# Optimization experiments

Hardware: AMD Instinct MI355X
Metric: run time of the kernel (lower is better)

The kernel has to match this reference:

```python
import jax, jax.numpy as jnp
import numpy as np

IMG, P, C = 512, 16, 1
D, DEPTH, H, DH, MLP = 768, 12, 8, 64, 2048
GRID = IMG // P          # 32
NP = GRID * GRID         # 1024 patches
N = NP + 1               # +cls token
EPS = 1e-5


def _ln(x, s, b):
    m = jnp.mean(x, -1, keepdims=True)
    v = jnp.mean((x - m) ** 2, -1, keepdims=True)
    return (x - m) * jax.lax.rsqrt(v + EPS) * s + b


def setup_inputs() -> dict:
    key = jax.random.key(0)
    ks = jax.random.split(key, 12)
    s = 0.02
    f32 = jnp.float32
    return {
        "x": jax.random.normal(ks[0], (4, C, IMG, IMG), f32),
        "conv_w": jax.random.normal(ks[1], (D, C, P, P), f32) * s,   # [out,in,kh,kw] like torch
        "conv_b": jnp.zeros((D,), f32),
        "cls_token": jax.random.normal(ks[2], (1, 1, D), f32),
        "pos_emb": jax.random.normal(ks[3], (1, N, D), f32),
        "qkv_w": jax.random.normal(ks[4], (DEPTH, D, 3 * H * DH), f32) * s,  # [in,out] layout
        "merge_w": jax.random.normal(ks[5], (DEPTH, H * DH, D), f32) * s,
        "merge_b": jnp.zeros((DEPTH, D), f32),
        "ln1_s": jnp.ones((DEPTH, D), f32),
        "ln1_b": jnp.zeros((DEPTH, D), f32),
        "ln2_s": jnp.ones((DEPTH, D), f32),
        "ln2_b": jnp.zeros((DEPTH, D), f32),
        "ffn_w1": jax.random.normal(ks[6], (DEPTH, D, MLP), f32) * s,
        "ffn_b1": jnp.zeros((DEPTH, MLP), f32),
        "ffn_w2": jax.random.normal(ks[7], (DEPTH, MLP, D), f32) * s,
        "ffn_b2": jnp.zeros((DEPTH, D), f32),
        "lnf_s": jnp.ones((D,), f32),
        "lnf_b": jnp.zeros((D,), f32),
    }


def reference(x, conv_w, conv_b, cls_token, pos_emb, qkv_w, merge_w, merge_b,
              ln1_s, ln1_b, ln2_s, ln2_b, ffn_w1, ffn_b1, ffn_w2, ffn_b2,
              lnf_s, lnf_b):
    B = x.shape[0]
    # Patch embed: stride-P conv == non-overlapping patch extraction + matmul
    xr = x.reshape(B, C, GRID, P, GRID, P)
    tok = jnp.einsum('bchpwq,dcpq->bhwd', xr, conv_w).reshape(B, NP, D) + conv_b
    t = jnp.concatenate([jnp.broadcast_to(cls_token, (B, 1, D)), tok], axis=1)
    t = t + pos_emb  # dropout is identity in eval
    scale = DH ** -0.5
    for i in range(DEPTH):
        # MSA with pre-LN
        h = _ln(t, ln1_s[i], ln1_b[i])
        qkv = (h @ qkv_w[i]).reshape(B, N, H, 3, DH)   # [B,N,H,3,DH]
        q = jnp.transpose(qkv[..., 0, :], (0, 2, 1, 3))  # [B,H,N,DH]
        k = jnp.transpose(qkv[..., 1, :], (0, 2, 1, 3))
        v = jnp.transpose(qkv[..., 2, :], (0, 2, 1, 3))
        att = jax.nn.softmax(jnp.einsum('bhnd,bhmd->bhnm', q, k) * scale, axis=-1)
        o = jnp.einsum('bhnm,bhmd->bhnd', att, v)
        o = jnp.transpose(o, (0, 2, 1, 3)).reshape(B, N, H * DH)
        t = t + (o @ merge_w[i] + merge_b[i])
        # FFN with pre-LN, exact (erf) GELU like torch nn.GELU
        h2 = _ln(t, ln2_s[i], ln2_b[i])
        f = jax.nn.gelu(h2 @ ffn_w1[i] + ffn_b1[i], approximate=False)
        t = t + (f @ ffn_w2[i] + ffn_b2[i])
    return _ln(t, lnf_s, lnf_b)
```

## Files before the change

kernel.cpp:

```cpp
#include <hip/hip_runtime.h>

#define DEV __device__ __forceinline__

typedef short s8v __attribute__((ext_vector_type(8)));
typedef float f4v __attribute__((ext_vector_type(4)));

DEV short f2bf(float f) {
  unsigned u = __float_as_uint(f);
  u += 0x7FFFu + ((u >> 16) & 1u);
  return (short)(u >> 16);
}
DEV short f2bf_fast(float f) {
  return (short)((__float_as_uint(f) + 0x8000u) >> 16);
}
DEV float bf2f(short s) { return __uint_as_float(((unsigned)(unsigned short)s) << 16); }

DEV void gld_lds16(const short* g, short* l) {
  __builtin_amdgcn_global_load_lds(
      (const __attribute__((address_space(1))) void*)g,
      (__attribute__((address_space(3))) void*)l, 16, 0, 0);
}

DEV int xcd_swz(int id, int nwg) {
  int q8 = nwg >> 3, r8 = nwg & 7, xcd = id & 7, off = id >> 3;
  return (xcd < r8) ? (xcd * (q8 + 1) + off) : (r8 * (q8 + 1) + (xcd - r8) * q8 + off);
}

template<int BN>
__global__ __launch_bounds__(256) void gemm_t(
    const short* __restrict__ A, const short* __restrict__ B, void* __restrict__ Cv,
    const float* __restrict__ bias,
    int M, int N, int K, int lda, int ldb, int ldc, int flags)
{
  constexpr int BPASS = BN / 32;
  constexpr int MI = (BN == 128) ? 4 : 2;
  __shared__ __align__(16) short As[2][64 * 64];
  __shared__ __align__(16) short Bs[2][BN * 64];
  int nwg = gridDim.x * gridDim.y;
  int idl = blockIdx.y * gridDim.x + blockIdx.x;
  int swz = xcd_swz(idl, nwg);
  int bx = swz % gridDim.x, by = swz / gridDim.x;
  int m0 = by * 64, n0 = bx * BN;
  int tid = threadIdx.x, lane = tid & 63, w = tid >> 6;
  int lr = lane & 15, kg = lane >> 4;
  int wrb = (BN == 128) ? 0 : (w >> 1) * 32;
  int wcb = (BN == 128) ? w * 32 : (w & 1) * 32;
  f4v acc[MI][2] = {};
  int NT = K >> 6;

#define STAGE(bufi, k0)                                                   \
  {                                                                       \
    _Pragma("unroll")                                                     \
    for (int p = 0; p < 2; ++p) {                                         \
      int ch = p * 256 + w * 64 + lane;                                   \
      int row = ch >> 3, c = (ch & 7) ^ (row & 7);                        \
      gld_lds16(A + (long)(m0 + row) * lda + (k0) + c * 8,                \
                &As[bufi][(p * 256 + w * 64) * 8]);                       \
    }                                                                     \
    _Pragma("unroll")                                                     \
    for (int p = 0; p < BPASS; ++p) {                                     \
      int ch = p * 256 + w * 64 + lane;                                   \
      int row = ch >> 3, c = (ch & 7) ^ (row & 7);                        \
      gld_lds16(B + (long)(n0 + row) * ldb + (k0) + c * 8,                \
                &Bs[bufi][(p * 256 + w * 64) * 8]);                       \
    }                                                                     \
  }

  STAGE(0, 0)
  for (int t = 0; t < NT; ++t) {
    int buf = t & 1;
    if (t + 1 < NT) {
      STAGE(buf ^ 1, (t + 1) * 64)
      if constexpr (BN == 128)
        asm volatile("s_waitcnt vmcnt(6)" ::: "memory");
      else
        asm volatile("s_waitcnt vmcnt(4)" ::: "memory");
    } else {
      asm volatile("s_waitcnt vmcnt(0)" ::: "memory");
    }
    __builtin_amdgcn_s_barrier();
    #pragma unroll
    for (int ks = 0; ks < 2; ++ks) {
      s8v av[MI], bv[2];
      #pragma unroll
      for (int mi = 0; mi < MI; ++mi) {
        int row = wrb + mi * 16 + lr;
        int sl = (ks * 4 + kg) ^ (row & 7);
        av[mi] = *(const s8v*)&As[buf][row * 64 + sl * 8];
      }
      #pragma unroll
      for (int ni = 0; ni < 2; ++ni) {
        int row = wcb + ni * 16 + lr;
        int sl = (ks * 4 + kg) ^ (row & 7);
        bv[ni] = *(const s8v*)&Bs[buf][row * 64 + sl * 8];
      }
      #pragma unroll
      for (int mi = 0; mi < MI; ++mi)
        #pragma unroll
        for (int ni = 0; ni < 2; ++ni)
          acc[mi][ni] = __builtin_amdgcn_mfma_f32_16x16x32_bf16(av[mi], bv[ni], acc[mi][ni], 0, 0, 0);
    }
    asm volatile("s_waitcnt lgkmcnt(0)" ::: "memory");
    __builtin_amdgcn_s_barrier();
  }
#undef STAGE

  float* Cf = (float*)Cv;
  short* Cb = (short*)Cv;
  #pragma unroll
  for (int mi = 0; mi < MI; ++mi)
    #pragma unroll
    for (int ni = 0; ni < 2; ++ni) {
      int col = n0 + wcb + ni * 16 + lr;
      float bvv = (flags & 1) ? bias[col] : 0.f;
      #pragma unroll
      for (int j = 0; j < 4; ++j) {
        int row = m0 + wrb + mi * 16 + kg * 4 + j;
        if (row >= M) continue;
        float v = acc[mi][ni][j] + bvv;
        if (flags & 2) v = 0.5f * v * (1.f + erff(v * 0.70710678118f));
        long ci = (long)row * ldc + col;
        if (flags & 8) Cb[ci] = f2bf(v);
        else { if (flags & 4) v += Cf[ci]; Cf[ci] = v; }
      }
    }
}

__global__ __launch_bounds__(256) void flash_k(
    const short* __restrict__ qkv, short* __restrict__ O)
{
  int swz = xcd_swz(blockIdx.x, 544);
  int z = swz / 17, qt = swz - z * 17;
  int zb = z >> 3, zh = z & 7;
  const short* base = qkv + (long)zb * 1025 * 1536 + zh * 192;
  const short* Qg = base;
  const short* Kg = base + 64;
  const short* Vg = base + 128;
  int q0 = qt * 64;
  int tid = threadIdx.x, lane = tid & 63, w = tid >> 6;
  int lr = lane & 15, kg = lane >> 4;

  __shared__ __align__(16) short Ks[2][64 * 64];
  __shared__ __align__(16) short Vt[2][64][72];

  s8v aq[2];
  {
    long qrow = q0 + w * 16 + lr;
    aq[0] = *(const s8v*)(Qg + qrow * 1536 + kg * 8);
    aq[1] = *(const s8v*)(Qg + qrow * 1536 + 32 + kg * 8);
  }

#define STAGE_K(bufi, kv0)                                                 \
  {                                                                        \
    int s0 = w * 128;                                                      \
    _Pragma("unroll")                                                      \
    for (int i = 0; i < 2; ++i) {                                          \
      int s = s0 + i * 64 + lane;                                          \
      int row = s >> 3, c = (s & 7) ^ (row & 7);                           \
      gld_lds16(Kg + (long)((kv0) + row) * 1536 + c * 8,                   \
                &Ks[bufi][(s0 + i * 64) * 8]);                             \
    }                                                                      \
  }

  f4v acc[4] = {};
  float m_run = -3.0e38f, l_run = 0.f;
  const float C2 = 0.18033688011112042f;

  STAGE_K(0, 0)
  #pragma unroll
  for (int p = 0; p < 2; ++p) {
    int s = p * 256 + tid;
    int key = s & 63, ch = s >> 6;
    s8v v = *(const s8v*)(Vg + (long)key * 1536 + ch * 8);
    #pragma unroll
    for (int j = 0; j < 8; ++j) Vt[0][ch * 8 + j][key] = v[j];
  }
  asm volatile("s_waitcnt vmcnt(0)" ::: "memory");
  asm volatile("s_waitcnt lgkmcnt(0)" ::: "memory");
  __builtin_amdgcn_s_barrier();

  for (int kt = 0; kt < 17; ++kt) {
    int cur = kt & 1;
    int kv0 = kt * 64;
    s8v vreg[2];
    int vok[2];
    if (kt < 16) {
      STAGE_K(cur ^ 1, kv0 + 64)
      #pragma unroll
      for (int p = 0; p < 2; ++p) {
        int s = p * 256 + tid;
        int key = (s & 63) + kv0 + 64, ch = s >> 6;
        vok[p] = key < 1025;
        vreg[p] = vok[p] ? *(const s8v*)(Vg + (long)key * 1536 + ch * 8) : s8v{};
      }
    }

    f4v sa[4] = {};
    __builtin_amdgcn_s_setprio(1);
    #pragma unroll
    for (int ni = 0; ni < 4; ++ni) {
      int row = ni * 16 + lr;
      #pragma unroll
      for (int ks = 0; ks < 2; ++ks) {
        int c = (ks * 4 + kg) ^ (row & 7);
        s8v kf = *(const s8v*)&Ks[cur][row * 64 + c * 8];
        sa[ni] = __builtin_amdgcn_mfma_f32_16x16x32_bf16(kf, aq[ks], sa[ni], 0, 0, 0);
      }
    }
    __builtin_amdgcn_s_setprio(0);

    float sv[4][4], pv[4][4];
    float tm = -3.0e38f;
    if (kt != 16) {
      #pragma unroll
      for (int ni = 0; ni < 4; ++ni)
        #pragma unroll
        for (int jj = 0; jj < 4; ++jj) {
          float s = sa[ni][jj] * C2;
          sv[ni][jj] = s;
          tm = fmaxf(tm, s);
        }
    } else {
      #pragma unroll
      for (int ni = 0; ni < 4; ++ni)
        #pragma unroll
        for (int jj = 0; jj < 4; ++jj) sv[ni][jj] = -3.0e38f;
      if (kg == 0) sv[0][0] = sa[0][0] * C2;
      tm = sv[0][0];
    }
    tm = fmaxf(tm, __shfl_xor(tm, 16));
    tm = fmaxf(tm, __shfl_xor(tm, 32));
    float m_new = fmaxf(m_run, tm);
    float scale = exp2f(m_run - m_new);
    m_run = m_new;
    float ts = 0.f;
    #pragma unroll
    for (int ni = 0; ni < 4; ++ni)
      #pragma unroll
      for (int jj = 0; jj < 4; ++jj) {
        float p = exp2f(sv[ni][jj] - m_new);
        pv[ni][jj] = p;
        ts += p;
      }
    ts += __shfl_xor(ts, 16);
    ts += __shfl_xor(ts, 32);
    l_run = l_run * scale + ts;

    float scq[4];
    #pragma unroll
    for (int jj = 0; jj < 4; ++jj)
      scq[jj] = __shfl(scale, kg * 4 + jj + 16 * kg);
    #pragma unroll
    for (int ni = 0; ni < 4; ++ni)
      #pragma unroll
      for (int jj = 0; jj < 4; ++jj) acc[ni][jj] *= scq[jj];

    if (kt < 16) {
      #pragma unroll
      for (int p = 0; p < 2; ++p) {
        int s = p * 256 + tid;
        int key = s & 63, ch = s >> 6;
        s8v v = vok[p] ? vreg[p] : s8v{};
        #pragma unroll
        for (int j = 0; j < 8; ++j) Vt[cur ^ 1][ch * 8 + j][key] = v[j];
      }
    }

    unsigned pr[4][2];
    #pragma unroll
    for (int ni = 0; ni < 4; ++ni)
      #pragma unroll
      for (int h = 0; h < 2; ++h) {
        unsigned lo = (unsigned)(unsigned short)f2bf_fast(pv[ni][2 * h]);
        unsigned hi = (unsigned)(unsigned short)f2bf_fast(pv[ni][2 * h + 1]);
        pr[ni][h] = lo | (hi << 16);
      }
    union PU { s8v v; unsigned u[4]; };
    PU apu[2];
    #pragma unroll
    for (int ks = 0; ks < 2; ++ks)
      #pragma unroll
      for (int t = 0; t < 4; ++t) {
        unsigned src = (kg & 2) ? pr[2 * ks + 1][t & 1] : pr[2 * ks][t & 1];
        apu[ks].u[t] = __shfl(src, lr + 16 * (2 * (kg & 1) + (t >> 1)));
      }

    __builtin_amdgcn_s_setprio(1);
    #pragma unroll
    for (int ni = 0; ni < 4; ++ni) {
      #pragma unroll
      for (int ks = 0; ks < 2; ++ks) {
        s8v bvv = *(const s8v*)&Vt[cur][ni * 16 + lr][ks * 32 + kg * 8];
        acc[ni] = __builtin_amdgcn_mfma_f32_16x16x32_bf16(apu[ks].v, bvv, acc[ni], 0, 0, 0);
      }
    }
    __builtin_amdgcn_s_setprio(0);
    asm volatile("s_waitcnt lgkmcnt(0)" ::: "memory");
    asm volatile("s_waitcnt vmcnt(0)" ::: "memory");
    __builtin_amdgcn_s_barrier();
  }
#undef STAGE_K

  float linv = 1.f / l_run;
  float invq[4];
  #pragma unroll
  for (int jj = 0; jj < 4; ++jj)
    invq[jj] = __shfl(linv, kg * 4 + jj + 16 * kg);
  #pragma unroll
  for (int ni = 0; ni < 4; ++ni)
    #pragma unroll
    for (int jj = 0; jj < 4; ++jj) {
      int row = q0 + w * 16 + kg * 4 + jj;
      if (row < 1025)
        O[((long)(zb * 1025 + row)) * 512 + zh * 64 + ni * 16 + lr] = f2bf(acc[ni][jj] * invq[jj]);
    }
}

DEV void tconv_body(const float* w, short* wt, int K, int N, int bx, int by, int tid)
{
  __shared__ float tile[32][33];
  int n0 = bx * 32, k0 = by * 32;
  int tx = tid & 31, ty = tid >> 5;
  #pragma unroll
  for (int j = 0; j < 4; ++j)
    tile[ty + j * 8][tx] = w[(long)(k0 + ty + j * 8) * N + n0 + tx];
  __syncthreads();
  #pragma unroll
  for (int j = 0; j < 4; ++j)
    wt[(long)(n0 + ty + j * 8) * K + k0 + tx] = f2bf(tile[tx][ty + j * 8]);
}

__global__ __launch_bounds__(256) void tconv4_k(
    const float* __restrict__ sq, const float* __restrict__ sm,
    const float* __restrict__ sf1, const float* __restrict__ sf2,
    short* __restrict__ dq, short* __restrict__ dm,
    short* __restrict__ df1, short* __restrict__ df2)
{
  int id = blockIdx.x, tid = threadIdx.x;
  if (id < 1152)       tconv_body(sq,  dq,  768, 1536, id % 48,          id / 48,          tid);
  else if (id < 1536)  tconv_body(sm,  dm,  512, 768,  (id - 1152) % 24, (id - 1152) / 24, tid);
  else if (id < 3072)  tconv_body(sf1, df1, 768, 2048, (id - 1536) % 64, (id - 1536) / 64, tid);
  else                 tconv_body(sf2, df2, 2048, 768, (id - 3072) % 24, (id - 3072) / 24, tid);
}

__global__ __launch_bounds__(256) void cvt_k(const float* __restrict__ in,
    short* __restrict__ out, int n)
{
  int i = blockIdx.x * 256 + threadIdx.x;
  if (i < n) out[i] = f2bf(in[i]);
}

DEV void st_ln(float* p, float v) { *p = v; }
DEV void st_ln(short* p, float v) { *p = f2bf(v); }

template<typename OT>
__global__ __launch_bounds__(256) void ln_k(const float* __restrict__ x,
    const float* __restrict__ g, const float* __restrict__ b,
    OT* __restrict__ y, int rows)
{
  int row = blockIdx.x;
  if (row >= rows) return;
  const float* xr = x + (long)row * 768;
  OT* yr = y + (long)row * 768;
  int t = threadIdx.x;
  float v0 = xr[t], v1 = xr[t + 256], v2 = xr[t + 512];
  float s = v0 + v1 + v2, s2 = v0 * v0 + v1 * v1 + v2 * v2;
  #pragma unroll
  for (int o = 32; o > 0; o >>= 1) { s += __shfl_down(s, o); s2 += __shfl_down(s2, o); }
  __shared__ float as_[4], as2_[4];
  if ((t & 63) == 0) { as_[t >> 6] = s; as2_[t >> 6] = s2; }
  __syncthreads();
  s = as_[0] + as_[1] + as_[2] + as_[3];
  s2 = as2_[0] + as2_[1] + as2_[2] + as2_[3];
  float mean = s * (1.f / 768.f);
  float var = s2 * (1.f / 768.f) - mean * mean;
  float r = rsqrtf(var + 1e-5f);
  st_ln(&yr[t],       (v0 - mean) * r * g[t]       + b[t]);
  st_ln(&yr[t + 256], (v1 - mean) * r * g[t + 256] + b[t + 256]);
  st_ln(&yr[t + 512], (v2 - mean) * r * g[t + 512] + b[t + 512]);
}

__global__ __launch_bounds__(256) void im2col_k(const float* __restrict__ x,
    short* __restrict__ A)
{
  int i = blockIdx.x * 256 + threadIdx.x;
  int k = i & 255, row = i >> 8;
  int px = k & 15, py = k >> 4;
  int gx = row & 31, gy = (row >> 5) & 31, b = row >> 10;
  A[i] = f2bf(x[((long)(b * 512) + gy * 16 + py) * 512 + gx * 16 + px]);
}

__global__ __launch_bounds__(256) void assemble_k(const short* __restrict__ tok,
    const float* __restrict__ cls, const float* __restrict__ pos, float* __restrict__ t)
{
  int i = blockIdx.x * 256 + threadIdx.x;
  int d = i % 768; int rn = i / 768; int n = rn % 1025; int b = rn / 1025;
  float v = (n == 0) ? cls[d] : bf2f(tok[((long)(b * 1024 + n - 1)) * 768 + d]);
  t[i] = v + pos[n * 768 + d];
}

extern "C" void kernel_launch(void* const* d_in, const int* in_sizes, int n_in,
                              void* d_out, int out_size, void* d_ws, size_t ws_size,
                              hipStream_t stream)
{
  const float* x       = (const float*)d_in[0];
  const float* conv_w  = (const float*)d_in[1];
  const float* conv_b  = (const float*)d_in[2];
  const float* cls     = (const float*)d_in[3];
  const float* pos     = (const float*)d_in[4];
  const float* qkv_w   = (const float*)d_in[5];
  const float* merge_w = (const float*)d_in[6];
  const float* merge_b = (const float*)d_in[7];
  const float* ln1_s   = (const float*)d_in[8];
  const float* ln1_b   = (const float*)d_in[9];
  const float* ln2_s   = (const float*)d_in[10];
  const float* ln2_b   = (const float*)d_in[11];
  const float* ffn_w1  = (const float*)d_in[12];
  const float* ffn_b1  = (const float*)d_in[13];
  const float* ffn_w2  = (const float*)d_in[14];
  const float* ffn_b2  = (const float*)d_in[15];
  const float* lnf_s   = (const float*)d_in[16];
  const float* lnf_b   = (const float*)d_in[17];

  char* wsp = (char*)d_ws;
  size_t o = 0;
  auto take = [&](size_t bytes) { char* r = wsp + o; o = (o + bytes + 255) & ~(size_t)255; return r; };
  short* wq   = (short*)take(1536ul * 768 * 2);
  short* wm   = (short*)take(768ul * 512 * 2);
  short* wf1  = (short*)take(2048ul * 768 * 2);
  short* wf2  = (short*)take(768ul * 2048 * 2);
  short* wcv  = (short*)take(768ul * 256 * 2);
  float* t    = (float*)take(4100ul * 768 * 4);
  char*  hO   = take(4352ul * 768 * 2);
  short* qkv  = (short*)take(4ul * 1025 * 1536 * 2);
  char*  fV   = take(4352ul * 2048 * 2);
  take(2ul << 20);

  short* h   = (short*)hO;
  short* O   = (short*)hO;
  short* f   = (short*)fV;
  short* imc = (short*)fV;
  short* tok = (short*)(fV + 4096ul * 256 * 2);

  dim3 blk(256);

  cvt_k<<<768, blk, 0, stream>>>(conv_w, wcv, 768 * 256);
  im2col_k<<<4096, blk, 0, stream>>>(x, imc);
  gemm_t<64><<<dim3(12, 64), blk, 0, stream>>>(imc, wcv, tok, conv_b,
      4096, 768, 256, 256, 256, 768, 1 | 8);
  assemble_k<<<12300, blk, 0, stream>>>(tok, cls, pos, t);

  for (int i = 0; i < 12; ++i) {
    tconv4_k<<<4608, blk, 0, stream>>>(
        qkv_w + (long)i * 768 * 1536, merge_w + (long)i * 512 * 768,
        ffn_w1 + (long)i * 768 * 2048, ffn_w2 + (long)i * 2048 * 768,
        wq, wm, wf1, wf2);

    ln_k<short><<<4100, blk, 0, stream>>>(t, ln1_s + i * 768, ln1_b + i * 768, h, 4100);
    gemm_t<128><<<dim3(12, 65), blk, 0, stream>>>(h, wq, qkv, nullptr,
        4100, 1536, 768, 768, 768, 1536, 8);
    flash_k<<<544, blk, 0, stream>>>(qkv, O);
    gemm_t<64><<<dim3(12, 65), blk, 0, stream>>>(O, wm, t, merge_b + i * 768,
        4100, 768, 512, 512, 512, 768, 1 | 4);
    ln_k<short><<<4100, blk, 0, stream>>>(t, ln2_s + i * 768, ln2_b + i * 768, h, 4100);
    gemm_t<128><<<dim3(16, 65), blk, 0, stream>>>(h, wf1, f, ffn_b1 + i * 2048,
        4100, 2048, 768, 768, 768, 2048, 1 | 2 | 8);
    gemm_t<64><<<dim3(12, 65), blk, 0, stream>>>(f, wf2, t, ffn_b2 + i * 768,
        4100, 768, 2048, 2048, 2048, 768, 1 | 4);
  }
  ln_k<float><<<4100, blk, 0, stream>>>(t, lnf_s, lnf_b, (float*)d_out, 4100);
}
```

Before: 2.134 ms.

## Stage V via async LDS loads with transpose reads and peel final key tile

```diff
diff --git a/kernel.cpp b/kernel.cpp
--- a/kernel.cpp
+++ b/kernel.cpp
@@ -4,6 +4,7 @@
 
 typedef short s8v __attribute__((ext_vector_type(8)));
 typedef float f4v __attribute__((ext_vector_type(4)));
+typedef unsigned int u32x2 __attribute__((ext_vector_type(2)));
 
 DEV short f2bf(float f) {
   unsigned u = __float_as_uint(f);
@@ -19,6 +20,12 @@
   __builtin_amdgcn_global_load_lds(
       (const __attribute__((address_space(1))) void*)g,
       (__attribute__((address_space(3))) void*)l, 16, 0, 0);
+}
+
+DEV u32x2 trr(unsigned lds_byte) {
+  u32x2 r;
+  asm volatile("ds_read_b64_tr_b16 %0, %1" : "=&v"(r) : "v"(lds_byte));
+  return r;
 }
 
 DEV int xcd_swz(int id, int nwg) {
@@ -141,7 +148,7 @@
   int lr = lane & 15, kg = lane >> 4;
 
   __shared__ __align__(16) short Ks[2][64 * 64];
-  __shared__ __align__(16) short Vt[2][64][72];
+  __shared__ __align__(16) short Vs[2][64 * 64];
 
   s8v aq[2];
   {
@@ -149,6 +156,10 @@
     aq[0] = *(const s8v*)(Qg + qrow * 1536 + kg * 8);
     aq[1] = *(const s8v*)(Qg + qrow * 1536 + 32 + kg * 8);
   }
+
+  unsigned vsbase = (unsigned)(unsigned long long)
+      (__attribute__((address_space(3))) void*)&Vs[0][0];
+  unsigned vtr = (unsigned)(lr * 8 + kg * 1024);
 
 #define STAGE_K(bufi, kv0)                                                 \
   {                                                                        \
@@ -161,38 +172,35 @@
                 &Ks[bufi][(s0 + i * 64) * 8]);                             \
     }                                                                      \
   }
+#define STAGE_V(bufi, kv0)                                                 \
+  {                                                                        \
+    int s0 = w * 128;                                                      \
+    _Pragma("unroll")                                                      \
+    for (int i = 0; i < 2; ++i) {                                          \
+      int ch = s0 + i * 64 + lane;                                         \
+      int st = ch >> 3, r = (ch & 7) >> 1, hh = ch & 1;                    \
+      int key = (kv0) + (st >> 2) * 4 + r;                                 \
+      int d = (st & 3) * 16 + hh * 8;                                      \
+      gld_lds16(Vg + (long)key * 1536 + d,                                 \
+                &Vs[bufi][(s0 + i * 64) * 8]);                             \
+    }                                                                      \
+  }
 
   f4v acc[4] = {};
   float m_run = -3.0e38f, l_run = 0.f;
   const float C2 = 0.18033688011112042f;
 
   STAGE_K(0, 0)
-  #pragma unroll
-  for (int p = 0; p < 2; ++p) {
-    int s = p * 256 + tid;
-    int key = s & 63, ch = s >> 6;
-    s8v v = *(const s8v*)(Vg + (long)key * 1536 + ch * 8);
-    #pragma unroll
-    for (int j = 0; j < 8; ++j) Vt[0][ch * 8 + j][key] = v[j];
-  }
+  STAGE_V(0, 0)
   asm volatile("s_waitcnt vmcnt(0)" ::: "memory");
-  asm volatile("s_waitcnt lgkmcnt(0)" ::: "memory");
   __builtin_amdgcn_s_barrier();
 
-  for (int kt = 0; kt < 17; ++kt) {
+  for (int kt = 0; kt < 16; ++kt) {
     int cur = kt & 1;
     int kv0 = kt * 64;
-    s8v vreg[2];
-    int vok[2];
-    if (kt < 16) {
+    if (kt < 15) {
       STAGE_K(cur ^ 1, kv0 + 64)
-      #pragma unroll
-      for (int p = 0; p < 2; ++p) {
-        int s = p * 256 + tid;
-        int key = (s & 63) + kv0 + 64, ch = s >> 6;
-        vok[p] = key < 1025;
-        vreg[p] = vok[p] ? *(const s8v*)(Vg + (long)key * 1536 + ch * 8) : s8v{};
-      }
+      STAGE_V(cur ^ 1, kv0 + 64)
     }
 
     f4v sa[4] = {};
@@ -211,23 +219,14 @@
 
     float sv[4][4], pv[4][4];
     float tm = -3.0e38f;
-    if (kt != 16) {
-      #pragma unroll
-      for (int ni = 0; ni < 4; ++ni)
-        #pragma unroll
-        for (int jj = 0; jj < 4; ++jj) {
-          float s = sa[ni][jj] * C2;
-          sv[ni][jj] = s;
-          tm = fmaxf(tm, s);
-        }
-    } else {
-      #pragma unroll
-      for (int ni = 0; ni < 4; ++ni)
-        #pragma unroll
-        for (int jj = 0; jj < 4; ++jj) sv[ni][jj] = -3.0e38f;
-      if (kg == 0) sv[0][0] = sa[0][0] * C2;
-      tm = sv[0][0];
-    }
+    #pragma unroll
+    for (int ni = 0; ni < 4; ++ni)
+      #pragma unroll
+      for (int jj = 0; jj < 4; ++jj) {
+        float s = sa[ni][jj] * C2;
+        sv[ni][jj] = s;
+        tm = fmaxf(tm, s);
+      }
     tm = fmaxf(tm, __shfl_xor(tm, 16));
     tm = fmaxf(tm, __shfl_xor(tm, 32));
     float m_new = fmaxf(m_run, tm);
@@ -255,17 +254,6 @@
       #pragma unroll
       for (int jj = 0; jj < 4; ++jj) acc[ni][jj] *= scq[jj];
 
-    if (kt < 16) {
-      #pragma unroll
-      for (int p = 0; p < 2; ++p) {
-        int s = p * 256 + tid;
-        int key = s & 63, ch = s >> 6;
-        s8v v = vok[p] ? vreg[p] : s8v{};
-        #pragma unroll
-        for (int j = 0; j < 8; ++j) Vt[cur ^ 1][ch * 8 + j][key] = v[j];
-      }
-    }
-
     unsigned pr[4][2];
     #pragma unroll
     for (int ni = 0; ni < 4; ++ni)
@@ -285,13 +273,27 @@
         apu[ks].u[t] = __shfl(src, lr + 16 * (2 * (kg & 1) + (t >> 1)));
       }
 
+    u32x2 tr[4][2][2];
+    unsigned vb = vsbase + (unsigned)cur * 8192u + vtr;
+    #pragma unroll
+    for (int ni = 0; ni < 4; ++ni)
+      #pragma unroll
+      for (int ks = 0; ks < 2; ++ks) {
+        tr[ni][ks][0] = trr(vb + ni * 128 + ks * 4096);
+        tr[ni][ks][1] = trr(vb + ni * 128 + ks * 4096 + 512);
+      }
+    asm volatile("s_waitcnt lgkmcnt(0)" ::: "memory");
+    __builtin_amdgcn_sched_barrier(0);
+
     __builtin_amdgcn_s_setprio(1);
     #pragma unroll
     for (int ni = 0; ni < 4; ++ni) {
       #pragma unroll
       for (int ks = 0; ks < 2; ++ks) {
-        s8v bvv = *(const s8v*)&Vt[cur][ni * 16 + lr][ks * 32 + kg * 8];
-        acc[ni] = __builtin_amdgcn_mfma_f32_16x16x32_bf16(apu[ks].v, bvv, acc[ni], 0, 0, 0);
+        union { s8v v; u32x2 u2[2]; } bb;
+        bb.u2[0] = tr[ni][ks][0];
+        bb.u2[1] = tr[ni][ks][1];
+        acc[ni] = __builtin_amdgcn_mfma_f32_16x16x32_bf16(apu[ks].v, bb.v, acc[ni], 0, 0, 0);
       }
     }
     __builtin_amdgcn_s_setprio(0);
@@ -300,6 +302,38 @@
     __builtin_amdgcn_s_barrier();
   }
 #undef STAGE_K
+#undef STAGE_V
+
+  {
+    s8v k0 = *(const s8v*)(Kg + 1024L * 1536 + kg * 8);
+    s8v k1 = *(const s8v*)(Kg + 1024L * 1536 + 32 + kg * 8);
+    float s = 0.f;
+    #pragma unroll
+    for (int j = 0; j < 8; ++j)
+      s += bf2f(aq[0][j]) * bf2f(k0[j]) + bf2f(aq[1][j]) * bf2f(k1[j]);
+    s += __shfl_xor(s, 16);
+    s += __shfl_xor(s, 32);
+    float sC = s * C2;
+    float m_new = fmaxf(m_run, sC);
+    float sc = exp2f(m_run - m_new);
+    float p = exp2f(sC - m_new);
+    l_run = l_run * sc + p;
+    float vrow[4];
+    #pragma unroll
+    for (int ni = 0; ni < 4; ++ni)
+      vrow[ni] = bf2f(Vg[1024L * 1536 + ni * 16 + lr]);
+    float scq[4], pq[4];
+    #pragma unroll
+    for (int jj = 0; jj < 4; ++jj) {
+      scq[jj] = __shfl(sc, kg * 4 + jj + 16 * kg);
+      pq[jj]  = __shfl(p,  kg * 4 + jj + 16 * kg);
+    }
+    #pragma unroll
+    for (int ni = 0; ni < 4; ++ni)
+      #pragma unroll
+      for (int jj = 0; jj < 4; ++jj)
+        acc[ni][jj] = acc[ni][jj] * scq[jj] + pq[jj] * vrow[ni];
+  }
 
   float linv = 1.f / l_run;
   float invq[4];
```

Result: no change. 2.096 ms (-1.8%).
